# Optimization experiments

Measured on AMD Instinct MI355X. Metric: run time of the kernel, lower is better.

Reference implementation:

```python
import jax, jax.numpy as jnp
import numpy as np

B, N, NY = 2, 4096, 4096
ENC_DIM, DEC_DIM, H = 768, 512, 8
HEAD_DIM = DEC_DIM // H
SCALE = HEAD_DIM ** -0.5


def setup_inputs() -> dict:
    key = jax.random.key(0)
    ks = jax.random.split(key, 8)
    lim_q = 1.0 / np.sqrt(DEC_DIM)
    lim_kv = 1.0 / np.sqrt(ENC_DIM)
    return {
        "x": jax.random.normal(ks[0], (B, N, DEC_DIM), jnp.float32),
        "y": jax.random.normal(ks[1], (B, NY, ENC_DIM), jnp.float32),
        "key_padding_mask": jax.random.randint(ks[2], (B, NY), 0, 2).astype(bool),
        "Wq": jax.random.uniform(ks[3], (DEC_DIM, DEC_DIM), jnp.float32, -lim_q, lim_q),
        "Wkv": jax.random.uniform(ks[4], (2 * DEC_DIM, ENC_DIM), jnp.float32, -lim_kv, lim_kv),
        "Wp": jax.random.uniform(ks[5], (DEC_DIM, DEC_DIM), jnp.float32, -lim_q, lim_q),
        "bp": jax.random.uniform(ks[6], (DEC_DIM,), jnp.float32, -lim_q, lim_q),
    }


def reference(x, y, key_padding_mask, Wq, Wkv, Wp, bp):
    # q projection: [B,N,C] -> [B,H,N,D]
    q = (x @ Wq.T).reshape(B, N, H, HEAD_DIM).transpose(0, 2, 1, 3)
    # kv projection: [B,Ny,E] -> [B,Ny,2C] -> k,v each [B,H,Ny,D]
    kv = (y @ Wkv.T).reshape(B, NY, 2, H, HEAD_DIM).transpose(2, 0, 3, 1, 4)
    k, v = kv[0], kv[1]
    # attention scores [B,H,N,Ny]
    attn = jnp.einsum("bhnd,bhmd->bhnm", q, k) * SCALE
    attn = jnp.where(key_padding_mask[:, None, None, :], -jnp.inf, attn)
    attn = jax.nn.softmax(attn, axis=-1)
    out = jnp.einsum("bhnm,bhmd->bhnd", attn, v)  # [B,H,N,D]
    out = out.transpose(0, 2, 1, 3).reshape(B, N, DEC_DIM)
    return out @ Wp.T + bp
```

## Files before the change

### kernel.cpp

```cpp
#include <hip/hip_runtime.h>
#include <hip/hip_bf16.h>
#include <stdint.h>

typedef __bf16 bf16_t;
typedef __bf16 bf16x8 __attribute__((ext_vector_type(8)));
typedef __bf16 bf16x4 __attribute__((ext_vector_type(4)));
typedef float  f32x4  __attribute__((ext_vector_type(4)));

#define MFMA16(a, b, c) __builtin_amdgcn_mfma_f32_16x16x32_bf16((a), (b), (c), 0, 0, 0)

__device__ __forceinline__ void gload_lds16(const void* g, void* l) {
  __builtin_amdgcn_global_load_lds((const __attribute__((address_space(1))) void*)g,
                                   (__attribute__((address_space(3))) void*)l, 16, 0, 0);
}

__device__ __forceinline__ void permlane32_swap(uint32_t& a, uint32_t& b) {
  asm("v_permlane32_swap_b32 %0, %1" : "+v"(a), "+v"(b));
}
__device__ __forceinline__ void permlane16_swap(uint32_t& a, uint32_t& b) {
  asm("v_permlane16_swap_b32 %0, %1" : "+v"(a), "+v"(b));
}

__device__ __forceinline__ uint32_t pack_e2(float a, float b) {
  union { bf16_t h[2]; uint32_t u; } p;
  p.h[0] = (bf16_t)__builtin_amdgcn_exp2f(a);
  p.h[1] = (bf16_t)__builtin_amdgcn_exp2f(b);
  return p.u;
}

#define QSCALE 0.18033688011112042f
#define NE_X   4194304UL
#define NE_Y   6291456UL
#define NE_WQ  262144UL
#define NE_WKV 786432UL
#define NE_WP  262144UL
#define NE_BP  512UL

__global__ void detect_and_mask(const uint16_t* __restrict__ xu,
                                const uint8_t* __restrict__ mk,
                                int* __restrict__ flags, bf16_t* __restrict__ mmul) {
  __shared__ int cbf, c3f1, c3f3, cnz;
  const int t = threadIdx.x;
  if (t == 0) { cbf = 0; c3f1 = 0; c3f3 = 0; cnz = 0; }
  __syncthreads();
  if (blockIdx.x == 0) {
    int local = 0;
    for (int i = t; i < 2048; i += 256) {
      uint16_t u = xu[2 * i];
      int e = (u >> 7) & 0xFF;
      if (u == 0 || (e >= 0x66 && e <= 0x88)) local++;
    }
    atomicAdd(&cbf, local);
  }
  int l1 = 0, l3 = 0, lnz = 0;
  for (int i = t; i < 4096; i += 256) {
    uint8_t b = mk[i];
    int p = i & 3;
    if (p == 1 && b == 0x3F) l1++;
    if (p == 3 && b == 0x3F) l3++;
    if (p != 0 && b != 0) lnz++;
  }
  atomicAdd(&c3f1, l1);
  atomicAdd(&c3f3, l3);
  atomicAdd(&cnz, lnz);
  __syncthreads();
  if (blockIdx.x == 0 && t == 0) flags[0] = (cbf > 1536) ? 1 : 0;
  const int fmt = (c3f1 > 0) ? 2 : (c3f3 > 0) ? 3 : (cnz > 0) ? 0 : 1;
  const int i = blockIdx.x * 256 + t;
  bool on;
  if (fmt == 0)      on = mk[i] != 0;
  else if (fmt == 1) on = ((const int*)mk)[i] != 0;
  else if (fmt == 2) on = (((const uint16_t*)mk)[i] & 0x7FFF) != 0;
  else               on = ((const float*)mk)[i] != 0.0f;
  mmul[i] = on ? (bf16_t)0.0f : (bf16_t)1.0f;
}

__global__ void convert_all(const void* __restrict__ x, const void* __restrict__ y,
                            const void* __restrict__ wq, const void* __restrict__ wkv,
                            const void* __restrict__ wp, const void* __restrict__ bp,
                            uint16_t* __restrict__ dst, const int* __restrict__ flags) {
  const size_t E0 = NE_X, E1 = E0 + NE_Y, E2 = E1 + NE_WQ, E3 = E2 + NE_WKV,
               E4 = E3 + NE_WP, E5 = E4 + NE_BP;
  size_t i8 = ((size_t)blockIdx.x * 256 + threadIdx.x) * 8;
  if (i8 >= E5) return;
  const void* src; size_t off;
  if      (i8 < E0) { src = x;   off = i8; }
  else if (i8 < E1) { src = y;   off = i8 - E0; }
  else if (i8 < E2) { src = wq;  off = i8 - E1; }
  else if (i8 < E3) { src = wkv; off = i8 - E2; }
  else if (i8 < E4) { src = wp;  off = i8 - E3; }
  else              { src = bp;  off = i8 - E4; }
  const bool isWq = (i8 >= E1 && i8 < E2);
  if (flags[0] && !isWq) {
    *(uint4*)(dst + i8) = *(const uint4*)((const uint16_t*)src + off);
    return;
  }
  float v[8];
  if (flags[0]) {
    const uint16_t* u = (const uint16_t*)src + off;
    for (int j = 0; j < 8; ++j) {
      union { uint32_t q; float f; } c; c.q = ((uint32_t)u[j]) << 16; v[j] = c.f;
    }
  } else {
    const float* f = (const float*)src + off;
    float4 a = *(const float4*)f;
    float4 b2 = *(const float4*)(f + 4);
    v[0] = a.x; v[1] = a.y; v[2] = a.z; v[3] = a.w;
    v[4] = b2.x; v[5] = b2.y; v[6] = b2.z; v[7] = b2.w;
  }
  const float sc = isWq ? QSCALE : 1.0f;
  union { bf16_t h[8]; uint4 u; } pk;
  for (int j = 0; j < 8; ++j) pk.h[j] = (bf16_t)(v[j] * sc);
  *(uint4*)(dst + i8) = pk.u;
}

template <int K, int MODE>
__launch_bounds__(256, 2)
__global__ void gemm_bt(const bf16_t* __restrict__ A, const bf16_t* __restrict__ W,
                        const bf16_t* __restrict__ bias, void* __restrict__ C,
                        bf16_t* __restrict__ Vt, const int* __restrict__ flags, int Ncols) {
  __shared__ __align__(16) char lds[16384];
  char* ldsA = lds;
  char* ldsW = lds + 8192;
  const int t = threadIdx.x;
  const int w = t >> 6, lane = t & 63, quad = lane >> 4, l16 = lane & 15;
  const int wr = w >> 1, wc = w & 1;
  const int m0 = blockIdx.y * 128, n0 = blockIdx.x * 128;

  f32x4 acc[4][4] = {};
  const int rowS = t >> 2, uS = t & 3;

  for (int k0 = 0; k0 < K; k0 += 32) {
    __syncthreads();
    for (int i = 0; i < 2; ++i) {
      int row = i * 64 + rowS;
      int c = uS ^ ((row >> 1) & 3);
      gload_lds16(A + (size_t)(m0 + row) * K + k0 + c * 8, ldsA + i * 4096 + w * 1024);
      gload_lds16(W + (size_t)(n0 + row) * K + k0 + c * 8, ldsW + i * 4096 + w * 1024);
    }
    __syncthreads();
    bf16x8 af[4], bfr[4];
    for (int mt = 0; mt < 4; ++mt) {
      int row = wr * 64 + mt * 16 + l16;
      int us = quad ^ ((row >> 1) & 3);
      af[mt] = *(const bf16x8*)(ldsA + row * 64 + us * 16);
    }
    for (int nt = 0; nt < 4; ++nt) {
      int row = wc * 64 + nt * 16 + l16;
      int us = quad ^ ((row >> 1) & 3);
      bfr[nt] = *(const bf16x8*)(ldsW + row * 64 + us * 16);
    }
    for (int mt = 0; mt < 4; ++mt)
      for (int nt = 0; nt < 4; ++nt)
        acc[mt][nt] = MFMA16(af[mt], bfr[nt], acc[mt][nt]);
  }

  const int mbase = m0 + wr * 64;
  for (int nt = 0; nt < 4; ++nt) {
    const int col = n0 + wc * 64 + nt * 16 + l16;
    if (MODE == 1 && col >= 512) {
      const int hd = col - 512;
      const int hh = hd >> 6, d = hd & 63;
      const int dt = d >> 4, l15 = d & 15;
      for (int mt = 0; mt < 4; ++mt) {
        int m = mbase + mt * 16 + quad * 4;
        int bb = m >> 12, keyg = m & 4095;
        int kt = keyg >> 6, keyin = keyg & 63;
        int kc = (keyin >> 5) & 1, jq = (keyin >> 3) & 3, j0 = keyin & 7;
        const bf16_t* mmp = bias + bb * 4096 + keyg;
        union { bf16_t h4[4]; uint2 u; } pk;
        for (int r = 0; r < 4; ++r) pk.h4[r] = (bf16_t)(acc[mt][nt][r] * (float)mmp[r]);
        size_t base = (((size_t)(bb * 8 + hh) * 64 + kt) * 8 + dt * 2 + kc) * 1024
                      + (jq * 16 + l15) * 16 + j0 * 2;
        *(uint2*)((char*)Vt + base) = pk.u;
      }
    } else if (MODE == 1) {
      for (int mt = 0; mt < 4; ++mt) {
        int m = mbase + mt * 16 + quad * 4;
        for (int r = 0; r < 4; ++r)
          ((bf16_t*)C)[(size_t)(m + r) * 512 + col] = (bf16_t)acc[mt][nt][r];
      }
    } else if (MODE == 0) {
      for (int mt = 0; mt < 4; ++mt) {
        int m = mbase + mt * 16 + quad * 4;
        for (int r = 0; r < 4; ++r)
          ((bf16_t*)C)[(size_t)(m + r) * Ncols + col] = (bf16_t)acc[mt][nt][r];
      }
    } else {
      const float bv = (float)bias[col];
      const bool obf = (flags[0] != 0);
      for (int mt = 0; mt < 4; ++mt) {
        int m = mbase + mt * 16 + quad * 4;
        for (int r = 0; r < 4; ++r) {
          float v = acc[mt][nt][r] + bv;
          if (obf) ((bf16_t*)C)[(size_t)(m + r) * Ncols + col] = (bf16_t)v;
          else     ((float*)C)[(size_t)(m + r) * Ncols + col] = v;
        }
      }
    }
  }
}

__launch_bounds__(256, 2)
__global__ void attn(const bf16_t* __restrict__ Qb, const bf16_t* __restrict__ Kb,
                     const bf16_t* __restrict__ Vfb, const bf16_t* __restrict__ mmul,
                     bf16_t* __restrict__ Ob) {
  const int t = threadIdx.x, w = t >> 6, lane = t & 63, quad = lane >> 4, l16 = lane & 15;
  const int bid = blockIdx.x;
  const int h = bid & 7;
  const int b = (bid >> 3) & 1;
  const int q0 = (bid >> 4) * 128;

  __shared__ __align__(16) char lds[65536];
  char* Qs = lds + 32768;

  for (int i = 0; i < 4; ++i) {
    int row = i * 32 + (t >> 3);
    int c = (t & 7) ^ (row & 7);
    gload_lds16(Qb + (size_t)(b * 4096 + q0 + row) * 512 + h * 64 + c * 8,
                Qs + i * 4096 + w * 1024);
  }
  for (int kt = 0; kt < 4; ++kt)
    for (int i = 0; i < 2; ++i) {
      int row = i * 32 + (t >> 3);
      int c = (t & 7) ^ (row & 7);
      gload_lds16(Kb + (size_t)(b * 4096 + kt * 64 + row) * 512 + h * 64 + c * 8,
                  lds + kt * 8192 + i * 4096 + w * 1024);
    }
  __syncthreads();

  bf16x8 qf[2][2];
  for (int ng = 0; ng < 2; ++ng)
    for (int kc = 0; kc < 2; ++kc) {
      int row = 32 * w + 16 * ng + l16;
      int u = (4 * kc + quad) ^ (row & 7);
      qf[ng][kc] = *(const bf16x8*)(Qs + row * 128 + u * 16);
    }
  __syncthreads();

  f32x4 o[2][4] = {};
  f32x4 lacc[2] = {};
  const char* Vfbase = (const char*)Vfb + (size_t)(b * 8 + h) * 524288;

  for (int ktg = 0; ktg < 16; ++ktg) {
    const int ktA = ktg * 4;
    if (ktg + 1 < 16) {
      for (int kk = 4; kk < 8; ++kk) {
        const int kt = ktA + kk;
        for (int i = 0; i < 2; ++i) {
          int row = i * 32 + (t >> 3);
          int c = (t & 7) ^ (row & 7);
          gload_lds16(Kb + (size_t)(b * 4096 + kt * 64 + row) * 512 + h * 64 + c * 8,
                      lds + (kt & 7) * 8192 + i * 4096 + w * 1024);
        }
      }
    }
#pragma unroll
    for (int kk = 0; kk < 4; ++kk) {
      const int kt = ktA + kk;
      const int kt0 = kt * 64;
      const char* Kl = lds + (kt & 7) * 8192;

      bf16x8 mf[2];
      mf[0] = *(const bf16x8*)(mmul + b * 4096 + kt0 + quad * 8);
      mf[1] = *(const bf16x8*)(mmul + b * 4096 + kt0 + 32 + quad * 8);
      const char* Vtile = Vfbase + (size_t)kt * 8192;
      bf16x8 vf[4][2];
      for (int dt = 0; dt < 4; ++dt)
        for (int kc = 0; kc < 2; ++kc)
          vf[dt][kc] = *(const bf16x8*)(Vtile + (dt * 2 + kc) * 1024 + lane * 16);

      bf16x8 kf[4][2];
      for (int mt = 0; mt < 4; ++mt)
        for (int kc = 0; kc < 2; ++kc) {
          int row = mt * 16 + l16;
          int u = (4 * kc + quad) ^ (row & 7);
          kf[mt][kc] = *(const bf16x8*)(Kl + row * 128 + u * 16);
        }

      bf16x8 pf[2][2];
      for (int ng = 0; ng < 2; ++ng) {
        f32x4 z[4];
        __builtin_amdgcn_s_setprio(1);
        for (int mt = 0; mt < 4; ++mt) {
          f32x4 zz = {};
          zz = MFMA16(kf[mt][0], qf[ng][0], zz);
          z[mt] = MFMA16(kf[mt][1], qf[ng][1], zz);
        }
        __builtin_amdgcn_s_setprio(0);
        uint32_t w0[4], w1[4];
        for (int mt = 0; mt < 4; ++mt) {
          w0[mt] = pack_e2(z[mt][0], z[mt][1]);
          w1[mt] = pack_e2(z[mt][2], z[mt][3]);
        }
        for (int kc = 0; kc < 2; ++kc) {
          uint32_t a0 = w0[2 * kc], b0 = w0[2 * kc + 1];
          uint32_t a1 = w1[2 * kc], b1 = w1[2 * kc + 1];
          permlane32_swap(a0, b0); permlane16_swap(a0, b0);
          permlane32_swap(a1, b1); permlane16_swap(a1, b1);
          union { uint32_t u[4]; bf16x8 v; } P;
          P.u[0] = a0; P.u[1] = a1; P.u[2] = b0; P.u[3] = b1;
          pf[ng][kc] = P.v;
        }
      }

      __builtin_amdgcn_s_setprio(1);
      for (int ng = 0; ng < 2; ++ng) {
        lacc[ng] = MFMA16(pf[ng][0], mf[0], lacc[ng]);
        lacc[ng] = MFMA16(pf[ng][1], mf[1], lacc[ng]);
      }
      for (int dt = 0; dt < 4; ++dt)
        for (int kc = 0; kc < 2; ++kc) {
          o[0][dt] = MFMA16(pf[0][kc], vf[dt][kc], o[0][dt]);
          o[1][dt] = MFMA16(pf[1][kc], vf[dt][kc], o[1][dt]);
        }
      __builtin_amdgcn_s_setprio(0);
    }
    __syncthreads();
  }

  for (int ng = 0; ng < 2; ++ng) {
    float inv[4];
    for (int r = 0; r < 4; ++r) inv[r] = 1.0f / lacc[ng][r];
    for (int dt = 0; dt < 4; ++dt)
      for (int r = 0; r < 4; ++r) {
        int q = q0 + 32 * w + 16 * ng + quad * 4 + r;
        int col = h * 64 + dt * 16 + l16;
        Ob[(size_t)(b * 4096 + q) * 512 + col] = (bf16_t)(o[ng][dt][r] * inv[r]);
      }
  }
}

extern "C" void kernel_launch(void* const* d_in, const int* in_sizes, int n_in,
                              void* d_out, int out_size, void* d_ws, size_t ws_size,
                              hipStream_t stream) {
  const void* x   = d_in[0];
  const void* y   = d_in[1];
  const void* msk = d_in[2];
  const void* Wq  = d_in[3];
  const void* Wkv = d_in[4];
  const void* Wp  = d_in[5];
  const void* bp  = d_in[6];

  char* ws = (char*)d_ws;
  bf16_t* Xb   = (bf16_t*)(ws + 0);
  bf16_t* Yb   = (bf16_t*)(ws + 8388608);
  bf16_t* Wqb  = (bf16_t*)(ws + 20971520);
  bf16_t* Wkvb = (bf16_t*)(ws + 21495808);
  bf16_t* Wpb  = (bf16_t*)(ws + 23068672);
  bf16_t* bpb  = (bf16_t*)(ws + 23592960);
  bf16_t* mmul = (bf16_t*)(ws + 23593984);
  int*    flags = (int*)(ws + 23610368);
  bf16_t* Kbuf  = (bf16_t*)(ws + 25165824);
  bf16_t* Vfrag = (bf16_t*)(ws + 33554432);
  bf16_t* Qbuf  = (bf16_t*)(ws + 8388608);
  bf16_t* Obuf  = (bf16_t*)(ws + 0);

  hipLaunchKernelGGL(detect_and_mask, dim3(32), dim3(256), 0, stream,
                     (const uint16_t*)x, (const uint8_t*)msk, flags, mmul);
  hipLaunchKernelGGL(convert_all, dim3(5761), dim3(256), 0, stream,
                     x, y, Wq, Wkv, Wp, bp, (uint16_t*)ws, flags);
  hipLaunchKernelGGL((gemm_bt<768, 1>), dim3(8, 64), dim3(256), 0, stream,
                     Yb, Wkvb, mmul, (void*)Kbuf, Vfrag, flags, 1024);
  hipLaunchKernelGGL((gemm_bt<512, 0>), dim3(4, 64), dim3(256), 0, stream,
                     Xb, Wqb, (const bf16_t*)nullptr, (void*)Qbuf, (bf16_t*)nullptr, flags, 512);
  hipLaunchKernelGGL(attn, dim3(512), dim3(256), 0, stream,
                     Qbuf, Kbuf, Vfrag, mmul, Obuf);
  hipLaunchKernelGGL((gemm_bt<512, 2>), dim3(4, 64), dim3(256), 0, stream,
                     Obuf, Wpb, bpb, d_out, (bf16_t*)nullptr, flags, 512);
}
```

Before: 245.3 us.

## Software-pipeline QK of next tile with softmax and PV of previous tile

Restructures the attention inner loop so the QK^T MFMAs for key tile kt are issued alongside the pack/permlane and PV MFMAs of tile kt-1, using ping-pong score buffers zA/zB plus a final drain step. The aim is to hide the dependency latency between the score MFMAs and the softmax/PV stage. The barrier moves to the top of each group iteration so the LDS slot being refilled is no longer read. The extra live score registers raise VGPR pressure, which may reduce occupancy.

New measurement: 245.9 us. No clear change (+0.2%).

```diff
diff --git a/kernel.cpp b/kernel.cpp
--- a/kernel.cpp
+++ b/kernel.cpp
@@ -240,10 +240,71 @@
 
   f32x4 o[2][4] = {};
   f32x4 lacc[2] = {};
+  f32x4 zA[2][4], zB[2][4];
   const char* Vfbase = (const char*)Vfb + (size_t)(b * 8 + h) * 524288;
+
+  auto load_kf = [&](bf16x8 (&kf)[4][2], int kt) {
+    const char* Kl = lds + (kt & 7) * 8192;
+    for (int mt = 0; mt < 4; ++mt)
+      for (int kc = 0; kc < 2; ++kc) {
+        int row = mt * 16 + l16;
+        int u = (4 * kc + quad) ^ (row & 7);
+        kf[mt][kc] = *(const bf16x8*)(Kl + row * 128 + u * 16);
+      }
+  };
+  auto qk = [&](f32x4 (&zN)[2][4], bf16x8 (&kf)[4][2]) {
+    __builtin_amdgcn_s_setprio(1);
+    for (int ng = 0; ng < 2; ++ng)
+      for (int mt = 0; mt < 4; ++mt) {
+        f32x4 zz = {};
+        zz = MFMA16(kf[mt][0], qf[ng][0], zz);
+        zN[ng][mt] = MFMA16(kf[mt][1], qf[ng][1], zz);
+      }
+    __builtin_amdgcn_s_setprio(0);
+  };
+  auto loadv = [&](bf16x8 (&vf)[4][2], bf16x8 (&mf)[2], int ktp) {
+    const int kt0 = ktp * 64;
+    mf[0] = *(const bf16x8*)(mmul + b * 4096 + kt0 + quad * 8);
+    mf[1] = *(const bf16x8*)(mmul + b * 4096 + kt0 + 32 + quad * 8);
+    const char* Vtile = Vfbase + (size_t)ktp * 8192;
+    for (int dt = 0; dt < 4; ++dt)
+      for (int kc = 0; kc < 2; ++kc)
+        vf[dt][kc] = *(const bf16x8*)(Vtile + (dt * 2 + kc) * 1024 + lane * 16);
+  };
+  auto softpv = [&](f32x4 (&zO)[2][4], bf16x8 (&vf)[4][2], bf16x8 (&mf)[2]) {
+    bf16x8 pf[2][2];
+    for (int ng = 0; ng < 2; ++ng) {
+      uint32_t w0[4], w1[4];
+      for (int mt = 0; mt < 4; ++mt) {
+        w0[mt] = pack_e2(zO[ng][mt][0], zO[ng][mt][1]);
+        w1[mt] = pack_e2(zO[ng][mt][2], zO[ng][mt][3]);
+      }
+      for (int kc = 0; kc < 2; ++kc) {
+        uint32_t a0 = w0[2 * kc], b0 = w0[2 * kc + 1];
+        uint32_t a1 = w1[2 * kc], b1 = w1[2 * kc + 1];
+        permlane32_swap(a0, b0); permlane16_swap(a0, b0);
+        permlane32_swap(a1, b1); permlane16_swap(a1, b1);
+        union { uint32_t u[4]; bf16x8 v; } P;
+        P.u[0] = a0; P.u[1] = a1; P.u[2] = b0; P.u[3] = b1;
+        pf[ng][kc] = P.v;
+      }
+    }
+    __builtin_amdgcn_s_setprio(1);
+    for (int ng = 0; ng < 2; ++ng) {
+      lacc[ng] = MFMA16(pf[ng][0], mf[0], lacc[ng]);
+      lacc[ng] = MFMA16(pf[ng][1], mf[1], lacc[ng]);
+    }
+    for (int dt = 0; dt < 4; ++dt)
+      for (int kc = 0; kc < 2; ++kc) {
+        o[0][dt] = MFMA16(pf[0][kc], vf[dt][kc], o[0][dt]);
+        o[1][dt] = MFMA16(pf[1][kc], vf[dt][kc], o[1][dt]);
+      }
+    __builtin_amdgcn_s_setprio(0);
+  };
 
   for (int ktg = 0; ktg < 16; ++ktg) {
     const int ktA = ktg * 4;
+    __syncthreads();
     if (ktg + 1 < 16) {
       for (int kk = 4; kk < 8; ++kk) {
         const int kt = ktA + kk;
@@ -258,65 +319,23 @@
 #pragma unroll
     for (int kk = 0; kk < 4; ++kk) {
       const int kt = ktA + kk;
-      const int kt0 = kt * 64;
-      const char* Kl = lds + (kt & 7) * 8192;
-
-      bf16x8 mf[2];
-      mf[0] = *(const bf16x8*)(mmul + b * 4096 + kt0 + quad * 8);
-      mf[1] = *(const bf16x8*)(mmul + b * 4096 + kt0 + 32 + quad * 8);
-      const char* Vtile = Vfbase + (size_t)kt * 8192;
-      bf16x8 vf[4][2];
-      for (int dt = 0; dt < 4; ++dt)
-        for (int kc = 0; kc < 2; ++kc)
-          vf[dt][kc] = *(const bf16x8*)(Vtile + (dt * 2 + kc) * 1024 + lane * 16);
-
-      bf16x8 kf[4][2];
-      for (int mt = 0; mt < 4; ++mt)
-        for (int kc = 0; kc < 2; ++kc) {
-          int row = mt * 16 + l16;
-          int u = (4 * kc + quad) ^ (row & 7);
-          kf[mt][kc] = *(const bf16x8*)(Kl + row * 128 + u * 16);
-        }
-
-      bf16x8 pf[2][2];
-      for (int ng = 0; ng < 2; ++ng) {
-        f32x4 z[4];
-        __builtin_amdgcn_s_setprio(1);
-        for (int mt = 0; mt < 4; ++mt) {
-          f32x4 zz = {};
-          zz = MFMA16(kf[mt][0], qf[ng][0], zz);
-          z[mt] = MFMA16(kf[mt][1], qf[ng][1], zz);
-        }
-        __builtin_amdgcn_s_setprio(0);
-        uint32_t w0[4], w1[4];
-        for (int mt = 0; mt < 4; ++mt) {
-          w0[mt] = pack_e2(z[mt][0], z[mt][1]);
-          w1[mt] = pack_e2(z[mt][2], z[mt][3]);
-        }
-        for (int kc = 0; kc < 2; ++kc) {
-          uint32_t a0 = w0[2 * kc], b0 = w0[2 * kc + 1];
-          uint32_t a1 = w1[2 * kc], b1 = w1[2 * kc + 1];
-          permlane32_swap(a0, b0); permlane16_swap(a0, b0);
-          permlane32_swap(a1, b1); permlane16_swap(a1, b1);
-          union { uint32_t u[4]; bf16x8 v; } P;
-          P.u[0] = a0; P.u[1] = a1; P.u[2] = b0; P.u[3] = b1;
-          pf[ng][kc] = P.v;
-        }
-      }
-
-      __builtin_amdgcn_s_setprio(1);
-      for (int ng = 0; ng < 2; ++ng) {
-        lacc[ng] = MFMA16(pf[ng][0], mf[0], lacc[ng]);
-        lacc[ng] = MFMA16(pf[ng][1], mf[1], lacc[ng]);
-      }
-      for (int dt = 0; dt < 4; ++dt)
-        for (int kc = 0; kc < 2; ++kc) {
-          o[0][dt] = MFMA16(pf[0][kc], vf[dt][kc], o[0][dt]);
-          o[1][dt] = MFMA16(pf[1][kc], vf[dt][kc], o[1][dt]);
-        }
-      __builtin_amdgcn_s_setprio(0);
-    }
-    __syncthreads();
+      const bool doC = (ktg + kk) > 0;
+      bf16x8 vf[4][2], mf[2], kf[4][2];
+      if (doC) loadv(vf, mf, kt - 1);
+      load_kf(kf, kt);
+      if (kk & 1) {
+        qk(zB, kf);
+        if (doC) softpv(zA, vf, mf);
+      } else {
+        qk(zA, kf);
+        if (doC) softpv(zB, vf, mf);
+      }
+    }
+  }
+  {
+    bf16x8 vf[4][2], mf[2];
+    loadv(vf, mf, 63);
+    softpv(zB, vf, mf);
   }
 
   for (int ng = 0; ng < 2; ++ng) {
```
